# Kernel tuning notes

Measured on AMD Instinct MI355X. Metric: run time of the kernel, lower is better.

Reference implementation:

```python
import jax, jax.numpy as jnp
import numpy as np

KS = 4                                  # kernel_size per axis
K = KS ** 3                             # 64 spatial filter bins
RADIUS = np.float32(1.5 * 6 * 0.025 / 2.0)   # filter_extent / 2 = 0.1125
N_REAL = 20000                          # fluid particles (index N_REAL = far dummy)
E_PAD = 1200000                         # padded edge count


def ball_to_cube(u):
    # volume-preserving unit-ball -> [-1,1]^3 cube map (Griepentrog et al., as in
    # Open3D-ML 'ball_to_cube_volume_preserving'): ball -> cylinder -> cube.
    eps = 1e-9
    x, y, z = u[..., 0], u[..., 1], u[..., 2]
    sq = x * x + y * y + z * z
    norm = jnp.sqrt(sq + eps)
    rxy2 = x * x + y * y
    polar = 1.25 * z * z > rxy2          # top/bottom cone region
    s = jnp.where(polar,
                  jnp.sqrt(3.0 * norm / (norm + jnp.abs(z) + eps)),
                  norm / jnp.sqrt(rxy2 + eps))
    xc = x * s
    yc = y * s
    zc = jnp.where(polar, jnp.sign(z) * norm, 1.5 * z)
    degen = sq < 1e-12
    xc = jnp.where(degen, 0.0, xc)
    yc = jnp.where(degen, 0.0, yc)
    zc = jnp.where(degen, 0.0, zc)
    # cylinder -> cube: inverse concentric (Shirley-Chiu) area-preserving map on xy
    r = jnp.sqrt(xc * xc + yc * yc + eps)
    c1 = jnp.abs(xc) >= jnp.abs(yc)
    xs = jnp.where(jnp.abs(xc) < eps, eps, xc)
    ys = jnp.where(jnp.abs(yc) < eps, eps, yc)
    fop = np.float32(4.0 / np.pi)
    a = jnp.where(c1, jnp.sign(xc) * r, jnp.sign(yc) * r * fop * jnp.arctan(xc / ys))
    b = jnp.where(c1, jnp.sign(xc) * r * fop * jnp.arctan(yc / xs), jnp.sign(yc) * r)
    tiny = (xc * xc + yc * yc) < 1e-12
    a = jnp.where(tiny, 0.0, a)
    b = jnp.where(tiny, 0.0, b)
    return jnp.stack([a, b, zc], axis=-1)


def cconv(feat, pos, src, dst, W, b):
    # ContinuousConv: normalize=False, align_corners=True, linear interpolation,
    # poly6 window on r^2/radius^2, self-neighbors excluded in the edge list.
    offs = (pos[dst] - pos[src]) / RADIUS              # (E,3), inside unit ball
    r2 = jnp.sum(offs * offs, axis=-1)
    win = jnp.clip((1.0 - r2) ** 3, 0.0, 1.0)          # window_poly6; 0 on pad edges
    g = jnp.clip((ball_to_cube(offs) * 0.5 + 0.5) * (KS - 1), 0.0, KS - 1)
    f0f = jnp.floor(g)
    t = g - f0f                                         # trilinear fractions
    f0 = f0f.astype(jnp.int32)
    fj = feat[dst] * win[:, None]                       # (E,Cin) windowed neighbor feats
    n = pos.shape[0]
    cin = feat.shape[1]
    B = jnp.zeros((n * K, cin), feat.dtype)             # per-query per-bin accumulator
    for c in range(8):                                  # 8 trilinear corners
        w = jnp.ones_like(r2)
        kf = jnp.zeros_like(src)
        for ax in range(3):
            bit = (c >> (2 - ax)) & 1
            ia = jnp.minimum(f0[:, ax] + bit, KS - 1)
            w = w * (t[:, ax] if bit else 1.0 - t[:, ax])
            kf = kf * KS + ia
        B = B + jax.ops.segment_sum(fj * w[:, None], src * K + kf, num_segments=n * K)
    out = jnp.einsum('nki,kio->no', B.reshape(n, K, cin), W.reshape(K, cin, -1))
    return out + b


def forward(pos, feats, edge_src, edge_dst, conv0_w, conv0_b, dense0_w, dense0_b,
            conv1_w, conv1_b, dense1_w, dense1_b, conv2_w, conv2_b, dense2_w, dense2_b,
            conv3_w, conv3_b, dense3_w, dense3_b):
    f = jnp.concatenate([jnp.ones_like(pos[:, :1]), feats], axis=-1)   # 13 channels
    x = jnp.concatenate([cconv(f, pos, edge_src, edge_dst, conv0_w, conv0_b),
                         f @ dense0_w + dense0_b], axis=-1)            # 64 + 32 = 96
    layers = [(conv1_w, conv1_b, dense1_w, dense1_b),
              (conv2_w, conv2_b, dense2_w, dense2_b),
              (conv3_w, conv3_b, dense3_w, dense3_b)]
    for cw, cb, dw, db in layers:
        inp = jax.nn.relu(x)
        y = cconv(inp, pos, edge_src, edge_dst, cw, cb) + inp @ dw + db
        x = (y + x) if y.shape[-1] == x.shape[-1] else y               # residual 64->64
    return (x * (1.0 / 128.0))[:N_REAL]                                # pos_correction


def setup_inputs() -> dict:
    rng = np.random.default_rng(0)
    spacing = 0.05                                  # 2 * particle_radius
    g = np.arange(28)
    pts = np.stack(np.meshgrid(g, g, g, indexing='ij'), -1).reshape(-1, 3).astype(np.float64) * spacing
    pts = pts[:N_REAL] + rng.uniform(-0.012, 0.012, (N_REAL, 3))
    # fixed-radius neighbor search, excluding self (radius_search_ignore_query_points)
    r2 = float(RADIUS) ** 2
    sq = (pts ** 2).sum(-1)
    src_l, dst_l = [], []
    for s in range(0, N_REAL, 1000):
        q = pts[s:s + 1000]
        d2 = (q ** 2).sum(-1)[:, None] + sq[None, :] - 2.0 * (q @ pts.T)
        ii, jj = np.nonzero(d2 < r2)
        ii = ii + s
        keep = ii != jj
        src_l.append(ii[keep])
        dst_l.append(jj[keep])
    src = np.concatenate(src_l).astype(np.int32)[:E_PAD]
    dst = np.concatenate(dst_l).astype(np.int32)[:E_PAD]
    pad = E_PAD - src.size
    src = np.concatenate([src, np.zeros(pad, np.int32)])
    dst = np.concatenate([dst, np.full(pad, N_REAL, np.int32)])   # edges to far dummy -> window 0
    pos = np.concatenate([pts, [[1e3, 1e3, 1e3]]], 0).astype(np.float32)
    key = jax.random.key(0)
    ks = jax.random.split(key, 12)
    def w(k, shape, fan_in):
        return jax.random.normal(k, shape, jnp.float32) * np.float32(1.0 / np.sqrt(fan_in))
    return {
        'pos': jnp.asarray(pos),
        'feats': jax.random.normal(ks[0], (N_REAL + 1, 12), jnp.float32),
        'edge_src': jnp.asarray(src),
        'edge_dst': jnp.asarray(dst),
        'conv0_w': w(ks[1], (KS, KS, KS, 13, 64), 13 * 27),
        'conv0_b': jnp.zeros((64,), jnp.float32),
        'dense0_w': w(ks[2], (13, 32), 13),
        'dense0_b': jnp.zeros((32,), jnp.float32),
        'conv1_w': w(ks[3], (KS, KS, KS, 96, 64), 96 * 27),
        'conv1_b': jnp.zeros((64,), jnp.float32),
        'dense1_w': w(ks[4], (96, 64), 96),
        'dense1_b': jnp.zeros((64,), jnp.float32),
        'conv2_w': w(ks[5], (KS, KS, KS, 64, 64), 64 * 27),
        'conv2_b': jnp.zeros((64,), jnp.float32),
        'dense2_w': w(ks[6], (64, 64), 64),
        'dense2_b': jnp.zeros((64,), jnp.float32),
        'conv3_w': w(ks[7], (KS, KS, KS, 64, 3), 64 * 27),
        'conv3_b': jnp.zeros((3,), jnp.float32),
        'dense3_w': w(ks[8], (64, 3), 64),
        'dense3_b': jnp.zeros((3,), jnp.float32),
    }


def reference(pos, feats, edge_src, edge_dst, conv0_w, conv0_b, dense0_w, dense0_b,
              conv1_w, conv1_b, dense1_w, dense1_b, conv2_w, conv2_b, dense2_w, dense2_b,
              conv3_w, conv3_b, dense3_w, dense3_b):
    return forward(pos, feats, edge_src, edge_dst, conv0_w, conv0_b, dense0_w, dense0_b,
                   conv1_w, conv1_b, dense1_w, dense1_b, conv2_w, conv2_b, dense2_w, dense2_b,
                   conv3_w, conv3_b, dense3_w, dense3_b)
```

## Files before the change

kernel.cpp:

```cpp
#include <hip/hip_runtime.h>
#include <math.h>

#define NPTS   20001
#define NREAL  20000
#define EPAD   1200000
#define KK     64
#define RADF   0.1125f

typedef _Float16 half8_t __attribute__((ext_vector_type(8)));
typedef float    floatx4 __attribute__((ext_vector_type(4)));

__device__ __forceinline__ float sgnf(float v){ return v>0.f ? 1.f : (v<0.f ? -1.f : 0.f); }

__global__ void k_find_ereal(const int* __restrict__ dst, int* __restrict__ ereal){
  int lo=0, hi=EPAD;
  while(lo<hi){ int mid=(lo+hi)>>1; if(dst[mid]==NREAL) hi=mid; else lo=mid+1; }
  *ereal = lo;
}

__global__ void k_csr(const int* __restrict__ src, const int* __restrict__ erealp,
                      int* __restrict__ row_start){
  int i = blockIdx.x*blockDim.x + threadIdx.x;
  if(i > NPTS) return;
  int E = *erealp;
  int lo=0, hi=E;
  while(lo<hi){ int mid=(lo+hi)>>1; if(src[mid] < i) lo=mid+1; else hi=mid; }
  row_start[i] = lo;
}

__global__ void k_build_f(const float* __restrict__ feats, float* __restrict__ f){
  int idx = blockIdx.x*blockDim.x + threadIdx.x;
  if(idx >= NPTS*13) return;
  int i = idx/13, c = idx - i*13;
  f[idx] = (c==0) ? 1.f : feats[i*12 + (c-1)];
}

__device__ __forceinline__ void edge_geom(float ox, float oy, float oz,
                                          float& win, float& t0, float& t1, float& t2, int& f0p){
  const float eps = 1e-9f;
  float sq = ox*ox + oy*oy + oz*oz;
  float u = 1.f - sq;
  win = fminf(fmaxf(u*u*u, 0.f), 1.f);
  float norm = sqrtf(sq + eps);
  float rxy2 = ox*ox + oy*oy;
  bool polar = (1.25f*oz*oz > rxy2);
  float s_p = sqrtf(3.f*norm/(norm + fabsf(oz) + eps));
  float s_n = norm / sqrtf(rxy2 + eps);
  float s = polar ? s_p : s_n;
  float xc = ox*s, yc = oy*s;
  float zc = polar ? sgnf(oz)*norm : 1.5f*oz;
  if(sq < 1e-12f){ xc = 0.f; yc = 0.f; zc = 0.f; }
  float r = sqrtf(xc*xc + yc*yc + eps);
  bool c1 = fabsf(xc) >= fabsf(yc);
  float xs = (fabsf(xc) < eps) ? eps : xc;
  float ys = (fabsf(yc) < eps) ? eps : yc;
  const float fop = 1.2732395447351628f;
  float a = c1 ? sgnf(xc)*r : sgnf(yc)*r*fop*atanf(xc/ys);
  float b = c1 ? sgnf(xc)*r*fop*atanf(yc/xs) : sgnf(yc)*r;
  if(xc*xc + yc*yc < 1e-12f){ a = 0.f; b = 0.f; }
  float g0 = fminf(fmaxf((a *0.5f+0.5f)*3.f, 0.f), 3.f);
  float g1 = fminf(fmaxf((b *0.5f+0.5f)*3.f, 0.f), 3.f);
  float g2 = fminf(fmaxf((zc*0.5f+0.5f)*3.f, 0.f), 3.f);
  float f00 = floorf(g0), f01 = floorf(g1), f02 = floorf(g2);
  t0 = g0 - f00; t1 = g1 - f01; t2 = g2 - f02;
  f0p = (int)f00 | ((int)f01 << 2) | ((int)f02 << 4);
}

__global__ __launch_bounds__(256) void k_geom(const float* __restrict__ pos,
    const int* __restrict__ esrc, const int* __restrict__ edst,
    float4* __restrict__ gw, int4* __restrict__ gmz)
{
  int e = blockIdx.x*blockDim.x + threadIdx.x;
  if(e >= EPAD) return;
  const int sn = esrc[e], d = edst[e];
  const float ox = (pos[d*3+0]-pos[sn*3+0])/RADF;
  const float oy = (pos[d*3+1]-pos[sn*3+1])/RADF;
  const float oz = (pos[d*3+2]-pos[sn*3+2])/RADF;
  float win, t0, t1, t2; int f0p;
  edge_geom(ox, oy, oz, win, t0, t1, t2, f0p);
  const int i0 = f0p & 3, i1 = (f0p>>2) & 3, i2 = f0p >> 4;
  const int X0 = i0 << 4, X1 = ((i0+1)&3) << 4;
  const int Y0 = i1 << 2, Y1 = ((i1+1)&3) << 2;
  const int Z0 = i2, Z1 = (i2+1) & 3;
  const float wx0 = win*(1.f-t0), wx1 = win*t0;
  const float wy0 = 1.f-t1, wy1 = t1;
  const float wz0 = 1.f-t2, wz1 = t2;
  gw[e] = make_float4(wx0*wy0, wx0*wy1, wx1*wy0, wx1*wy1);
  const int p0 = Z0 & 1;
  const float zA = p0 ? wz1 : wz0;
  const int   cA = p0 ? Z1 : Z0;
  const int   cB = p0 ? Z0 : Z1;
  const int cells0 = (X0|Y0|cA) | ((X0|Y1|cA)<<8) | ((X1|Y0|cA)<<16) | ((X1|Y1|cA)<<24);
  const int cells1 = (X0|Y0|cB) | ((X0|Y1|cB)<<8) | ((X1|Y0|cB)<<16) | ((X1|Y1|cB)<<24);
  gmz[e] = make_int4(__float_as_int(zA), cells0, cells1, d);
}

template<int RELU, int OUT3>
__global__ __launch_bounds__(128) void k_scat64(
    const float* __restrict__ feat, const float4* __restrict__ gw,
    const int4* __restrict__ gmz, const int* __restrict__ row_start,
    float* __restrict__ B, int node_base,
    const float* __restrict__ W3, float* __restrict__ out)
{
  constexpr int BSZ = 64*64;
  __shared__ __align__(16) float Bl[BSZ];
  __shared__ __align__(16) float4 Sgw[64];
  __shared__ __align__(16) int4   Smd[64];
  __shared__ float red[8];
  const int tid  = threadIdx.x;
  const int node = node_base + blockIdx.x;

  for(int j = tid*4; j < BSZ; j += 512)
    *(float4*)&Bl[j] = make_float4(0.f,0.f,0.f,0.f);

  const int e0 = row_start[node], e1 = row_start[node+1];
  const int wv   = tid >> 6;
  const int lane = tid & 63;
  const int g    = (tid >> 4) & 3;
  const int f4   = (tid & 15) * 4;
  const int gsh  = g * 8;
  const bool g01 = (g < 2), g02 = (g & 1) == 0;

  for(int eb = e0; eb < e1; eb += 64){
    const int n = (e1 - eb < 64) ? (e1 - eb) : 64;
    __syncthreads();
    if(lane < n){
      if(wv == 0) Sgw[lane] = gw[eb + lane];
      else        Smd[lane] = gmz[eb + lane];
    }
    __syncthreads();
    #pragma unroll 4
    for(int i = 0; i < n; ++i){
      const float4 q  = Sgw[i];
      const int4   md = Smd[i];
      const float zA = __int_as_float(md.x);
      const float z  = wv ? (1.f - zA) : zA;
      const int   cp = wv ? md.z : md.y;
      float4 v = *(const float4*)(feat + (size_t)md.w*64 + f4);
      if(RELU){
        v.x = fmaxf(v.x, 0.f); v.y = fmaxf(v.y, 0.f);
        v.z = fmaxf(v.z, 0.f); v.w = fmaxf(v.w, 0.f);
      }
      const int   cell = (cp >> gsh) & 255;
      const float qa = g01 ? q.x : q.z;
      const float qb = g01 ? q.y : q.w;
      const float w  = (g02 ? qa : qb) * z;
      float4* p = (float4*)&Bl[(cell << 6) + f4];
      float4 o = *p;
      o.x = fmaf(w, v.x, o.x); o.y = fmaf(w, v.y, o.y);
      o.z = fmaf(w, v.z, o.z); o.w = fmaf(w, v.w, o.w);
      *p = o;
    }
  }
  __syncthreads();

  if(!OUT3){
    float* Bg = B + (size_t)blockIdx.x*BSZ;
    for(int j = tid*4; j < BSZ; j += 512)
      *(float4*)&Bg[j] = *(const float4*)&Bl[j];
  } else {
    float s0=0.f, s1=0.f, s2=0.f;
    for(int j = tid; j < BSZ; j += 128){
      float v = Bl[j];
      s0 = fmaf(v, W3[j*3+0], s0);
      s1 = fmaf(v, W3[j*3+1], s1);
      s2 = fmaf(v, W3[j*3+2], s2);
    }
    #pragma unroll
    for(int off = 32; off > 0; off >>= 1){
      s0 += __shfl_down(s0, off);
      s1 += __shfl_down(s1, off);
      s2 += __shfl_down(s2, off);
    }
    if((tid & 63) == 0){
      red[wv*4+0] = s0; red[wv*4+1] = s1; red[wv*4+2] = s2;
    }
    __syncthreads();
    if(tid == 0 && node < NREAL){
      out[node*3+0] += (red[0]+red[4])*(1.f/128.f);
      out[node*3+1] += (red[1]+red[5])*(1.f/128.f);
      out[node*3+2] += (red[2]+red[6])*(1.f/128.f);
    }
  }
}

template<int RELU>
__global__ __launch_bounds__(128) void k_scat96(
    const float* __restrict__ feat, const float4* __restrict__ gw,
    const int4* __restrict__ gmz, const int* __restrict__ row_start,
    float* __restrict__ B, int node_base)
{
  constexpr int CIN = 96, BSZ = KK*CIN, NP = 48;
  __shared__ __align__(16) float Bl[BSZ];
  const int tid  = threadIdx.x;
  const int node = node_base + blockIdx.x;

  for(int j = tid*4; j < BSZ; j += 512)
    *(float4*)&Bl[j] = make_float4(0.f,0.f,0.f,0.f);

  const int e0 = row_start[node], e1 = row_start[node+1];
  const int wv   = tid >> 6;
  const int lane = tid & 63;
  const bool act = (lane < NP);
  float2* Bp2 = (float2*)Bl;
  __syncthreads();

  if(act){
    #pragma unroll 2
    for(int e = e0; e < e1; ++e){
      const float4 q  = gw[e];
      const int4   md = gmz[e];
      const float zA = __int_as_float(md.x);
      const float z  = wv ? (1.f - zA) : zA;
      const int   cp = wv ? md.z : md.y;
      float2 v2 = ((const float2*)(feat + (size_t)md.w*CIN))[lane];
      if(RELU){ v2.x = fmaxf(v2.x,0.f); v2.y = fmaxf(v2.y,0.f); }
      v2.x *= z; v2.y *= z;
      const int b0 = ( cp        & 255)*NP + lane;
      const int b1 = ((cp >> 8)  & 255)*NP + lane;
      const int b2 = ((cp >> 16) & 255)*NP + lane;
      const int b3 = (((unsigned)cp) >> 24)*NP + lane;
      float2 o0 = Bp2[b0], o1 = Bp2[b1], o2 = Bp2[b2], o3 = Bp2[b3];
      o0.x = fmaf(q.x, v2.x, o0.x); o0.y = fmaf(q.x, v2.y, o0.y);
      o1.x = fmaf(q.y, v2.x, o1.x); o1.y = fmaf(q.y, v2.y, o1.y);
      o2.x = fmaf(q.z, v2.x, o2.x); o2.y = fmaf(q.z, v2.y, o2.y);
      o3.x = fmaf(q.w, v2.x, o3.x); o3.y = fmaf(q.w, v2.y, o3.y);
      Bp2[b0] = o0; Bp2[b1] = o1; Bp2[b2] = o2; Bp2[b3] = o3;
    }
  }
  __syncthreads();

  float* Bg = B + (size_t)blockIdx.x*BSZ;
  for(int j = tid*4; j < BSZ; j += 512)
    *(float4*)&Bg[j] = *(const float4*)&Bl[j];
}

__global__ __launch_bounds__(128) void k_scat13(
    const float* __restrict__ feat, const float4* __restrict__ gw,
    const int4* __restrict__ gmz, const int* __restrict__ row_start,
    float* __restrict__ B, int node_base)
{
  constexpr int CIN = 13, BSZ = KK*CIN, ESW = 4, CSTRIDE = BSZ + 8;
  __shared__ __align__(16) float Bl[ESW*CSTRIDE];
  const int tid  = threadIdx.x;
  const int node = node_base + blockIdx.x;

  for(int j = tid; j < ESW*CSTRIDE; j += 128) Bl[j] = 0.f;

  const int e0 = row_start[node], e1 = row_start[node+1];
  const int wv   = tid >> 6;
  const int lane = tid & 63;
  const int slot = lane >> 4;
  const int c    = lane & 15;
  const bool act = (c < CIN);
  float* Bp = Bl + slot*CSTRIDE;
  __syncthreads();

  if(act){
    for(int e = e0 + slot; e < e1; e += ESW){
      const float4 q  = gw[e];
      const int4   md = gmz[e];
      const float zA = __int_as_float(md.x);
      const float z  = wv ? (1.f - zA) : zA;
      const int   cp = wv ? md.z : md.y;
      float v = feat[(size_t)md.w*CIN + c] * z;
      const int b0 = ( cp        & 255)*CIN + c;
      const int b1 = ((cp >> 8)  & 255)*CIN + c;
      const int b2 = ((cp >> 16) & 255)*CIN + c;
      const int b3 = (((unsigned)cp) >> 24)*CIN + c;
      float o0 = Bp[b0], o1 = Bp[b1], o2 = Bp[b2], o3 = Bp[b3];
      o0 = fmaf(q.x, v, o0); o1 = fmaf(q.y, v, o1);
      o2 = fmaf(q.z, v, o2); o3 = fmaf(q.w, v, o3);
      Bp[b0] = o0; Bp[b1] = o1; Bp[b2] = o2; Bp[b3] = o3;
    }
  }
  __syncthreads();

  float* Bg = B + (size_t)blockIdx.x*BSZ;
  for(int j = tid*4; j < BSZ; j += 512){
    float4 a = *(const float4*)&Bl[j];
    #pragma unroll
    for(int k = 1; k < ESW; ++k){
      const float4 t = *(const float4*)&Bl[k*CSTRIDE + j];
      a.x += t.x; a.y += t.y; a.z += t.z; a.w += t.w;
    }
    *(float4*)&Bg[j] = a;
  }
}

__global__ void k_cvtW(const float* __restrict__ W, _Float16* __restrict__ WhT,
                       _Float16* __restrict__ WlT, int Kd)
{
  int idx = blockIdx.x*blockDim.x + threadIdx.x;
  if(idx >= 64*Kd) return;
  int o = idx / Kd, k = idx - o*Kd;
  float w = W[(size_t)k*64 + o];
  _Float16 h = (_Float16)w;
  WhT[idx] = h;
  WlT[idx] = (_Float16)(w - (float)h);
}

__global__ __launch_bounds__(256) void k_gemm_mfma(
    const float* __restrict__ A, const _Float16* __restrict__ WhT,
    const _Float16* __restrict__ WlT, float* __restrict__ P,
    int M, int Kd, int node_base, int ksteps_per)
{
  __shared__ __align__(16) _Float16 Ah[64][40];
  __shared__ __align__(16) _Float16 Al[64][40];
  __shared__ __align__(16) _Float16 Bh[64][40];
  __shared__ __align__(16) _Float16 Blo[64][40];
  const int tid = threadIdx.x;
  const int mbase = blockIdx.x * 64;
  const int s = blockIdx.y;
  const int kt0 = s * ksteps_per * 32;
  const int kt1 = min(Kd, kt0 + ksteps_per*32);
  const int wv = tid >> 6, lane = tid & 63;
  const int row  = tid >> 2;
  const int kseg = (tid & 3) * 8;
  const int frow = lane & 15, fk = (lane >> 4) * 8;

  floatx4 acc[4];
  #pragma unroll
  for(int c=0;c<4;++c){ acc[c][0]=0.f; acc[c][1]=0.f; acc[c][2]=0.f; acc[c][3]=0.f; }

  const int grow = mbase + row;
  const float* Arow = (grow < M) ? (A + (size_t)grow*Kd) : nullptr;
  const _Float16* WhRow = WhT + (size_t)row*Kd;
  const _Float16* WlRow = WlT + (size_t)row*Kd;

  for(int kt = kt0; kt < kt1; kt += 32){
    float av[8];
    if(Arow){
      *(float4*)&av[0] = *(const float4*)(Arow + kt + kseg);
      *(float4*)&av[4] = *(const float4*)(Arow + kt + kseg + 4);
    } else {
      #pragma unroll
      for(int j=0;j<8;++j) av[j] = 0.f;
    }
    half8_t hv, lv;
    #pragma unroll
    for(int j=0;j<8;++j){
      _Float16 h = (_Float16)av[j];
      hv[j] = h;
      lv[j] = (_Float16)(av[j] - (float)h);
    }
    half8_t wh = *(const half8_t*)(WhRow + kt + kseg);
    half8_t wl = *(const half8_t*)(WlRow + kt + kseg);
    __syncthreads();
    *(half8_t*)&Ah[row][kseg]  = hv;
    *(half8_t*)&Al[row][kseg]  = lv;
    *(half8_t*)&Bh[row][kseg]  = wh;
    *(half8_t*)&Blo[row][kseg] = wl;
    __syncthreads();
    const half8_t ah = *(const half8_t*)&Ah[wv*16 + frow][fk];
    const half8_t al = *(const half8_t*)&Al[wv*16 + frow][fk];
    #pragma unroll
    for(int c=0;c<4;++c){
      const half8_t bh = *(const half8_t*)&Bh[c*16 + frow][fk];
      const half8_t bl = *(const half8_t*)&Blo[c*16 + frow][fk];
      acc[c] = __builtin_amdgcn_mfma_f32_16x16x32_f16(ah, bh, acc[c], 0, 0, 0);
      acc[c] = __builtin_amdgcn_mfma_f32_16x16x32_f16(al, bh, acc[c], 0, 0, 0);
      acc[c] = __builtin_amdgcn_mfma_f32_16x16x32_f16(ah, bl, acc[c], 0, 0, 0);
    }
  }

  const int prow0 = mbase + wv*16 + (lane>>4)*4;
  const int pcol  = lane & 15;
  #pragma unroll
  for(int c=0;c<4;++c){
    #pragma unroll
    for(int r=0;r<4;++r){
      const int rr = prow0 + r;
      if(rr < M)
        P[((size_t)s*NPTS + node_base + rr)*64 + c*16 + pcol] = acc[c][r];
    }
  }
}

template<int S>
__global__ void k_combine(const float* __restrict__ P, float* __restrict__ x,
                          int ldout, int colofs)
{
  int idx = blockIdx.x*blockDim.x + threadIdx.x;
  if(idx >= NPTS*16) return;
  int node = idx >> 4, c4 = (idx & 15) * 4;
  float4 s = *(const float4*)(P + (size_t)node*64 + c4);
  #pragma unroll
  for(int k=1;k<S;++k){
    float4 t = *(const float4*)(P + ((size_t)k*NPTS + node)*64 + c4);
    s.x+=t.x; s.y+=t.y; s.z+=t.z; s.w+=t.w;
  }
  float* xp = x + (size_t)node*ldout + colofs + c4;
  float4 o = *(float4*)xp;
  o.x+=s.x; o.y+=s.y; o.z+=s.z; o.w+=s.w;
  *(float4*)xp = o;
}

__global__ void k_dense0(const float* __restrict__ f, const float* __restrict__ dW,
                         const float* __restrict__ db, const float* __restrict__ cb0,
                         float* __restrict__ out)
{
  int idx = blockIdx.x*blockDim.x + threadIdx.x;
  if(idx >= NPTS*96) return;
  int i = idx/96, c = idx - i*96;
  if(c < 64){ out[idx] = cb0[c]; return; }
  int o = c - 64;
  float s = db[o];
  const float* row = f + (size_t)i*13;
  #pragma unroll
  for(int j=0;j<13;++j) s = fmaf(row[j], dW[j*32+o], s);
  out[idx] = s;
}

__global__ void k_dense(const float* __restrict__ in, int cin,
                        const float* __restrict__ dW, const float* __restrict__ db,
                        const float* __restrict__ cb, const float* __restrict__ resid,
                        float* __restrict__ out)
{
  int idx = blockIdx.x*blockDim.x + threadIdx.x;
  if(idx >= NPTS*64) return;
  int i = idx >> 6, o = idx & 63;
  float s = db[o] + cb[o];
  if(resid) s += resid[idx];
  const float* row = in + (size_t)i*cin;
  for(int c=0;c<cin;++c) s = fmaf(fmaxf(row[c],0.f), dW[c*64+o], s);
  out[idx] = s;
}

__global__ void k_dense3(const float* __restrict__ x2, const float* __restrict__ dW,
                         const float* __restrict__ db, const float* __restrict__ cb,
                         float* __restrict__ out)
{
  int idx = blockIdx.x*blockDim.x + threadIdx.x;
  if(idx >= NREAL*3) return;
  int i = idx/3, o = idx - i*3;
  float s = db[o] + cb[o];
  const float* row = x2 + (size_t)i*64;
  for(int c=0;c<64;++c) s = fmaf(fmaxf(row[c],0.f), dW[c*3+o], s);
  out[idx] = s * (1.f/128.f);
}

static inline size_t alup(size_t x){ return (x + 255) & ~(size_t)255; }

static inline int calc_rows(size_t bcap, int cin, int want){
  size_t perrow = (size_t)KK * cin * 4;
  size_t r = (perrow > 0) ? bcap / perrow : 0;
  if(r >= (size_t)want) return want;
  r = (r / 128) * 128;
  if(r < 128) r = 128;
  return (int)r;
}

extern "C" void kernel_launch(void* const* d_in, const int* in_sizes, int n_in,
                              void* d_out, int out_size, void* d_ws, size_t ws_size,
                              hipStream_t stream)
{
  const float* pos   = (const float*)d_in[0];
  const float* feats = (const float*)d_in[1];
  const int*   esrc  = (const int*)d_in[2];
  const int*   edst  = (const int*)d_in[3];
  const float* c0w = (const float*)d_in[4];
  const float* c0b = (const float*)d_in[5];
  const float* d0w = (const float*)d_in[6];
  const float* d0b = (const float*)d_in[7];
  const float* c1w = (const float*)d_in[8];
  const float* c1b = (const float*)d_in[9];
  const float* d1w = (const float*)d_in[10];
  const float* d1b = (const float*)d_in[11];
  const float* c2w = (const float*)d_in[12];
  const float* c2b = (const float*)d_in[13];
  const float* d2w = (const float*)d_in[14];
  const float* d2b = (const float*)d_in[15];
  const float* c3w = (const float*)d_in[16];
  const float* c3b = (const float*)d_in[17];
  const float* d3w = (const float*)d_in[18];
  const float* d3b = (const float*)d_in[19];
  float* out = (float*)d_out;

  char* w = (char*)d_ws;
  size_t off = 0;
  float* f  = (float*)(w+off); off += alup((size_t)NPTS*13*4);
  float* x0 = (float*)(w+off); off += alup((size_t)NPTS*96*4);
  float* x1 = (float*)(w+off); off += alup((size_t)NPTS*64*4);
  float* x2 = (float*)(w+off); off += alup((size_t)NPTS*64*4);
  int* row_start = (int*)(w+off); off += alup((size_t)(NPTS+1)*4);
  int* ereal = (int*)(w+off);     off += alup(16);
  float4* gw = (float4*)(w+off);  off += alup((size_t)EPAD*16);
  int4*  gmz = (int4*)(w+off);    off += alup((size_t)EPAD*16);
  float* P  = (float*)(w+off); off += alup((size_t)8*NPTS*64*4);
  _Float16* whT = (_Float16*)(w+off); off += alup((size_t)64*6144*2);
  _Float16* wlT = (_Float16*)(w+off); off += alup((size_t)64*6144*2);
  float* B = (float*)(w+off);
  size_t bcap = (ws_size > off) ? (ws_size - off) : 0;

  k_find_ereal<<<1,1,0,stream>>>(edst, ereal);
  k_csr<<<(NPTS+1+255)/256,256,0,stream>>>(esrc, ereal, row_start);
  k_build_f<<<(NPTS*13+255)/256,256,0,stream>>>(feats, f);
  k_geom<<<(EPAD+255)/256,256,0,stream>>>(pos, esrc, edst, gw, gmz);

  k_dense0<<<(NPTS*96+255)/256,256,0,stream>>>(f, d0w, d0b, c0b, x0);
  {
    k_cvtW<<<(64*832+255)/256,256,0,stream>>>(c0w, whT, wlT, 832);
    int rows = calc_rows(bcap, 13, 8192);
    for(int base = 0; base < NPTS; base += rows){
      int m = (NPTS - base < rows) ? (NPTS - base) : rows;
      k_scat13<<<m,128,0,stream>>>(f, gw, gmz, row_start, B, base);
      k_gemm_mfma<<<dim3((m+63)/64, 8),256,0,stream>>>(B, whT, wlT, P, m, 832, base, 4);
    }
    k_combine<8><<<(NPTS*16+255)/256,256,0,stream>>>(P, x0, 96, 0);
  }

  k_dense<<<(NPTS*64+255)/256,256,0,stream>>>(x0, 96, d1w, d1b, c1b, nullptr, x1);
  {
    k_cvtW<<<(64*6144+255)/256,256,0,stream>>>(c1w, whT, wlT, 6144);
    int rows = calc_rows(bcap, 96, 4096);
    for(int base = 0; base < NPTS; base += rows){
      int m = (NPTS - base < rows) ? (NPTS - base) : rows;
      k_scat96<1><<<m,128,0,stream>>>(x0, gw, gmz, row_start, B, base);
      k_gemm_mfma<<<dim3((m+63)/64, 8),256,0,stream>>>(B, whT, wlT, P, m, 6144, base, 24);
    }
    k_combine<8><<<(NPTS*16+255)/256,256,0,stream>>>(P, x1, 64, 0);
  }

  k_dense<<<(NPTS*64+255)/256,256,0,stream>>>(x1, 64, d2w, d2b, c2b, x1, x2);
  {
    k_cvtW<<<(64*4096+255)/256,256,0,stream>>>(c2w, whT, wlT, 4096);
    int rows = calc_rows(bcap, 64, 4096);
    for(int base = 0; base < NPTS; base += rows){
      int m = (NPTS - base < rows) ? (NPTS - base) : rows;
      k_scat64<1,0><<<m,128,0,stream>>>(x1, gw, gmz, row_start, B, base, nullptr, nullptr);
      k_gemm_mfma<<<dim3((m+63)/64, 8),256,0,stream>>>(B, whT, wlT, P, m, 4096, base, 16);
    }
    k_combine<8><<<(NPTS*16+255)/256,256,0,stream>>>(P, x2, 64, 0);
  }

  k_dense3<<<(NREAL*3+255)/256,256,0,stream>>>(x2, d3w, d3b, c3b, out);
  k_scat64<1,1><<<NPTS,128,0,stream>>>(x2, gw, gmz, row_start, nullptr, 0, c3w, out);
}
```

Before: 1.084 ms.

## Rewrite 64-channel edge scatter as split-fp16 MFMA over per-chunk weight matrices

```diff
diff --git a/kernel.cpp b/kernel.cpp
--- a/kernel.cpp
+++ b/kernel.cpp
@@ -96,71 +96,111 @@
 }
 
 template<int RELU, int OUT3>
-__global__ __launch_bounds__(128) void k_scat64(
+__global__ __launch_bounds__(256) void k_scat64m(
     const float* __restrict__ feat, const float4* __restrict__ gw,
     const int4* __restrict__ gmz, const int* __restrict__ row_start,
     float* __restrict__ B, int node_base,
     const float* __restrict__ W3, float* __restrict__ out)
 {
-  constexpr int BSZ = 64*64;
-  __shared__ __align__(16) float Bl[BSZ];
-  __shared__ __align__(16) float4 Sgw[64];
-  __shared__ __align__(16) int4   Smd[64];
-  __shared__ float red[8];
+  __shared__ __align__(16) _Float16 Wh[64][40];
+  __shared__ __align__(16) _Float16 Wl[64][40];
+  __shared__ __align__(16) _Float16 Fh[64][40];
+  __shared__ __align__(16) _Float16 Fl[64][40];
+  __shared__ float Bl[OUT3 ? 4096 : 4];
+  __shared__ float red[16];
+
   const int tid  = threadIdx.x;
   const int node = node_base + blockIdx.x;
-
-  for(int j = tid*4; j < BSZ; j += 512)
-    *(float4*)&Bl[j] = make_float4(0.f,0.f,0.f,0.f);
-
-  const int e0 = row_start[node], e1 = row_start[node+1];
   const int wv   = tid >> 6;
   const int lane = tid & 63;
-  const int g    = (tid >> 4) & 3;
-  const int f4   = (tid & 15) * 4;
-  const int gsh  = g * 8;
-  const bool g01 = (g < 2), g02 = (g & 1) == 0;
-
-  for(int eb = e0; eb < e1; eb += 64){
-    const int n = (e1 - eb < 64) ? (e1 - eb) : 64;
-    __syncthreads();
-    if(lane < n){
-      if(wv == 0) Sgw[lane] = gw[eb + lane];
-      else        Smd[lane] = gmz[eb + lane];
-    }
-    __syncthreads();
-    #pragma unroll 4
-    for(int i = 0; i < n; ++i){
-      const float4 q  = Sgw[i];
-      const int4   md = Smd[i];
-      const float zA = __int_as_float(md.x);
-      const float z  = wv ? (1.f - zA) : zA;
-      const int   cp = wv ? md.z : md.y;
-      float4 v = *(const float4*)(feat + (size_t)md.w*64 + f4);
-      if(RELU){
-        v.x = fmaxf(v.x, 0.f); v.y = fmaxf(v.y, 0.f);
-        v.z = fmaxf(v.z, 0.f); v.w = fmaxf(v.w, 0.f);
+  const int frow = lane & 15, fk = (lane >> 4) * 8;
+
+  floatx4 acc[4];
+  #pragma unroll
+  for(int nt=0;nt<4;++nt){ acc[nt][0]=0.f; acc[nt][1]=0.f; acc[nt][2]=0.f; acc[nt][3]=0.f; }
+
+  half8_t hz;
+  #pragma unroll
+  for(int q8=0;q8<8;++q8) hz[q8] = (_Float16)0;
+
+  const int e0 = row_start[node], e1 = row_start[node+1];
+
+  for(int eb = e0; eb < e1; eb += 32){
+    const int n = (e1 - eb < 32) ? (e1 - eb) : 32;
+    __syncthreads();
+    float4 q; int4 md;
+    if(wv == 0 && lane < 32){
+      int ei = eb + lane; if(ei >= e1) ei = e1 - 1;
+      q  = gw[ei];
+      md = gmz[ei];
+    }
+    for(int j = tid; j < 320; j += 256){
+      ((half8_t*)Wh)[j] = hz;
+      ((half8_t*)Wl)[j] = hz;
+    }
+    {
+      half8_t hreg, lreg;
+      #pragma unroll
+      for(int j=0;j<8;++j){
+        int ej = eb + wv*8 + j; if(ej >= e1) ej = e1 - 1;
+        const int dst = gmz[ej].w;
+        float v = feat[(size_t)dst*64 + lane];
+        if(RELU) v = fmaxf(v, 0.f);
+        _Float16 h = (_Float16)v;
+        hreg[j] = h;
+        lreg[j] = (_Float16)(v - (float)h);
       }
-      const int   cell = (cp >> gsh) & 255;
-      const float qa = g01 ? q.x : q.z;
-      const float qb = g01 ? q.y : q.w;
-      const float w  = (g02 ? qa : qb) * z;
-      float4* p = (float4*)&Bl[(cell << 6) + f4];
-      float4 o = *p;
-      o.x = fmaf(w, v.x, o.x); o.y = fmaf(w, v.y, o.y);
-      o.z = fmaf(w, v.z, o.z); o.w = fmaf(w, v.w, o.w);
-      *p = o;
-    }
-  }
-  __syncthreads();
+      *(half8_t*)&Fh[lane][wv*8] = hreg;
+      *(half8_t*)&Fl[lane][wv*8] = lreg;
+    }
+    __syncthreads();
+    if(wv == 0 && lane < n){
+      const float zA = __int_as_float(md.x), zB = 1.f - zA;
+      #pragma unroll
+      for(int t=0;t<8;++t){
+        const int   cells = (t < 4) ? md.y : md.z;
+        const float zz    = (t < 4) ? zA : zB;
+        const int   cell  = (cells >> ((t & 3) * 8)) & 255;
+        const float qq    = ((t&3)==0) ? q.x : ((t&3)==1) ? q.y : ((t&3)==2) ? q.z : q.w;
+        const float wgt   = qq * zz;
+        const _Float16 h  = (_Float16)wgt;
+        Wh[cell][lane] = h;
+        Wl[cell][lane] = (_Float16)(wgt - (float)h);
+      }
+    }
+    __syncthreads();
+    const half8_t ah = *(const half8_t*)&Wh[wv*16 + frow][fk];
+    const half8_t al = *(const half8_t*)&Wl[wv*16 + frow][fk];
+    #pragma unroll
+    for(int nt=0; nt<4; ++nt){
+      const half8_t bh = *(const half8_t*)&Fh[nt*16 + frow][fk];
+      const half8_t bl = *(const half8_t*)&Fl[nt*16 + frow][fk];
+      acc[nt] = __builtin_amdgcn_mfma_f32_16x16x32_f16(ah, bh, acc[nt], 0, 0, 0);
+      acc[nt] = __builtin_amdgcn_mfma_f32_16x16x32_f16(al, bh, acc[nt], 0, 0, 0);
+      acc[nt] = __builtin_amdgcn_mfma_f32_16x16x32_f16(ah, bl, acc[nt], 0, 0, 0);
+    }
+  }
 
   if(!OUT3){
-    float* Bg = B + (size_t)blockIdx.x*BSZ;
-    for(int j = tid*4; j < BSZ; j += 512)
-      *(float4*)&Bg[j] = *(const float4*)&Bl[j];
+    float* Bg = B + (size_t)blockIdx.x*4096;
+    #pragma unroll
+    for(int nt=0;nt<4;++nt)
+      #pragma unroll
+      for(int r=0;r<4;++r){
+        const int cell = wv*16 + (lane>>4)*4 + r;
+        Bg[cell*64 + nt*16 + (lane&15)] = acc[nt][r];
+      }
   } else {
+    #pragma unroll
+    for(int nt=0;nt<4;++nt)
+      #pragma unroll
+      for(int r=0;r<4;++r){
+        const int cell = wv*16 + (lane>>4)*4 + r;
+        Bl[cell*64 + nt*16 + (lane&15)] = acc[nt][r];
+      }
+    __syncthreads();
     float s0=0.f, s1=0.f, s2=0.f;
-    for(int j = tid; j < BSZ; j += 128){
+    for(int j = tid; j < 4096; j += 256){
       float v = Bl[j];
       s0 = fmaf(v, W3[j*3+0], s0);
       s1 = fmaf(v, W3[j*3+1], s1);
@@ -172,14 +212,14 @@
       s1 += __shfl_down(s1, off);
       s2 += __shfl_down(s2, off);
     }
-    if((tid & 63) == 0){
+    if(lane == 0){
       red[wv*4+0] = s0; red[wv*4+1] = s1; red[wv*4+2] = s2;
     }
     __syncthreads();
     if(tid == 0 && node < NREAL){
-      out[node*3+0] += (red[0]+red[4])*(1.f/128.f);
-      out[node*3+1] += (red[1]+red[5])*(1.f/128.f);
-      out[node*3+2] += (red[2]+red[6])*(1.f/128.f);
+      out[node*3+0] += (red[0]+red[4]+red[8] +red[12])*(1.f/128.f);
+      out[node*3+1] += (red[1]+red[5]+red[9] +red[13])*(1.f/128.f);
+      out[node*3+2] += (red[2]+red[6]+red[10]+red[14])*(1.f/128.f);
     }
   }
 }
@@ -528,12 +568,12 @@
     int rows = calc_rows(bcap, 64, 4096);
     for(int base = 0; base < NPTS; base += rows){
       int m = (NPTS - base < rows) ? (NPTS - base) : rows;
-      k_scat64<1,0><<<m,128,0,stream>>>(x1, gw, gmz, row_start, B, base, nullptr, nullptr);
+      k_scat64m<1,0><<<m,256,0,stream>>>(x1, gw, gmz, row_start, B, base, nullptr, nullptr);
       k_gemm_mfma<<<dim3((m+63)/64, 8),256,0,stream>>>(B, whT, wlT, P, m, 4096, base, 16);
     }
     k_combine<8><<<(NPTS*16+255)/256,256,0,stream>>>(P, x2, 64, 0);
   }
 
   k_dense3<<<(NREAL*3+255)/256,256,0,stream>>>(x2, d3w, d3b, c3b, out);
-  k_scat64<1,1><<<NPTS,128,0,stream>>>(x2, gw, gmz, row_start, nullptr, 0, c3w, out);
-}
+  k_scat64m<1,1><<<NPTS,256,0,stream>>>(x2, gw, gmz, row_start, nullptr, 0, c3w, out);
+}
```

Measured after the change: 1.061 ms. 2.0% less time.
